# Kernel tuning notes

Hardware: AMD Instinct MI355X
Metric: run time of the kernel (lower is better)

## Reference

```python
import jax, jax.numpy as jnp
import numpy as np

N = 262144          # ray samples
L = 16              # grid levels
T = 2 ** 19         # hash table entries per level
F = 2               # features per entry
NMIN, NMAX = 16, 2048
SB = 1.0            # scene_bound
DW, CW = 64, 64     # density / color MLP widths

_PRIMES = jnp.array([1, 2654435761, 805459861], dtype=jnp.uint32)
_OFFS = jnp.asarray(np.stack(np.meshgrid([0, 1], [0, 1], [0, 1], indexing='ij'), -1).reshape(8, 3), dtype=jnp.uint32)  # 8 cube corners


def _scalings():
    g = np.exp((np.log(NMAX) - np.log(NMIN)) / (L - 1))
    return jnp.asarray(np.floor(NMIN * g ** np.arange(L)), dtype=jnp.float32)  # (L,)


def hash_encode(pos01, table):
    # pos01: (N,3) in [0,1]; table: (L*T, F)
    scaled = pos01[:, None, :] * _scalings()[None, :, None]        # (N,L,3)
    floor = jnp.floor(scaled)
    frac = scaled - floor                                          # (N,L,3)
    corners = floor.astype(jnp.uint32)[:, :, None, :] + _OFFS[None, None]  # (N,L,8,3)
    h = corners * _PRIMES                                          # uint32 wraparound hashing
    idx = (h[..., 0] ^ h[..., 1] ^ h[..., 2]) % jnp.uint32(T)      # (N,L,8)
    idx = idx.astype(jnp.int32) + (jnp.arange(L, dtype=jnp.int32) * T)[None, :, None]
    feats = table[idx]                                             # (N,L,8,F) gather
    sel = _OFFS.astype(bool)[None, None]                           # (1,1,8,3)
    w = jnp.prod(jnp.where(sel, frac[:, :, None, :], 1.0 - frac[:, :, None, :]), axis=-1)  # (N,L,8)
    out = jnp.einsum('nlcf,nlc->nlf', feats, w)                    # trilinear interp
    return out.reshape(out.shape[0], L * F)                        # (N, 32)


def sh_encode(d):
    # 4th-order real spherical harmonics, 16 components (instant-ngp convention)
    x, y, z = d[..., 0], d[..., 1], d[..., 2]
    xx, yy, zz = x * x, y * y, z * z
    xy, yz, xz = x * y, y * z, x * z
    return jnp.stack([
        jnp.full_like(x, 0.28209479177387814),
        -0.48860251190291987 * y,
        0.48860251190291987 * z,
        -0.48860251190291987 * x,
        1.0925484305920792 * xy,
        -1.0925484305920792 * yz,
        0.94617469575755997 * zz - 0.31539156525252005,
        -1.0925484305920792 * xz,
        0.54627421529603959 * (xx - yy),
        0.59004358992664352 * y * (-3.0 * xx + yy),
        2.8906114426405538 * xy * z,
        0.45704579946446572 * y * (1.0 - 5.0 * zz),
        0.3731763325901154 * z * (5.0 * zz - 3.0),
        0.45704579946446572 * x * (1.0 - 5.0 * zz),
        1.445305721320277 * z * (xx - yy),
        0.59004358992664352 * x * (xx - 3.0 * yy),
    ], axis=-1)  # (N,16)


def setup_inputs() -> dict:
    key = jax.random.key(0)
    ks = jax.random.split(key, 10)
    position = jax.random.uniform(ks[0], (N, 3), jnp.float32, -SB, SB)
    d = jax.random.normal(ks[1], (N, 3), jnp.float32)
    direction = d / jnp.linalg.norm(d, axis=-1, keepdims=True)
    hash_table = jax.random.uniform(ks[2], (L * T, F), jnp.float32, -1e-4, 1e-4)
    def dense(k, fin, fout, std):
        return (jax.random.normal(k, (fin, fout), jnp.float32) * std,
                jnp.zeros((fout,), jnp.float32))
    w1, b1 = dense(ks[3], L * F, DW, 0.01)      # normal() init in source
    w2, b2 = dense(ks[4], DW, 16, 0.01)
    w3, b3 = dense(ks[5], 16 + 16, CW, 0.01)
    w4, b4 = dense(ks[6], CW, CW, 0.01)
    w5, b5 = dense(ks[7], CW, 3, 0.1)           # default lecun-ish scale
    return dict(position=position, direction=direction, hash_table=hash_table,
                w1=w1, b1=b1, w2=w2, b2=b2, w3=w3, b3=b3, w4=w4, b4=b4, w5=w5, b5=b5)


def reference(position, direction, hash_table, w1, b1, w2, b2, w3, b3, w4, b4, w5, b5):
    p = (position + SB) / (2.0 * SB)                 # -> [0,1]
    enc = hash_encode(p, hash_table)                 # (N,32)
    h = jax.nn.relu(enc @ w1 + b1)                   # density MLP
    h = h @ w2 + b2                                  # (N,16)
    density = jnp.exp(h[:, 0:1])                     # exponential_density_activation
    sh = sh_encode(direction)                        # (N,16)
    c = jnp.concatenate([h, sh], axis=-1)            # (N,32)
    c = jax.nn.relu(c @ w3 + b3)
    c = jax.nn.relu(c @ w4 + b4)
    c = c @ w5 + b5
    color = jax.nn.sigmoid(c)                        # high_dynamic_range=False
    return jnp.concatenate([density, color], axis=-1)  # (N,4) drgbs
```

## Files before the change

### kernel.cpp

```cpp
#include <hip/hip_runtime.h>
#include <cmath>

namespace {
constexpr int kN = 262144;
constexpr int kL = 16;
constexpr int kT = 1 << 19;
constexpr unsigned kTMask = kT - 1;

typedef __attribute__((ext_vector_type(8))) short short8;
typedef __attribute__((ext_vector_type(4))) float f32x4;
typedef __attribute__((ext_vector_type(4))) unsigned short ushort4v;

struct Scales { float s[kL]; };

__device__ __forceinline__ unsigned short f2bf(float f) {
    unsigned u = __builtin_bit_cast(unsigned, f);
    return (unsigned short)((u + 0x7FFFu + ((u >> 16) & 1u)) >> 16);
}

__global__ __launch_bounds__(256) void prep_w(
    const float* __restrict__ w1, const float* __restrict__ w2,
    const float* __restrict__ w3, const float* __restrict__ w4,
    const float* __restrict__ w5, unsigned short* __restrict__ out)
{
    const int i = blockIdx.x * 256 + threadIdx.x;
    const int f = i >> 9;
    const int l = (i >> 3) & 63;
    const int e = i & 7;
    const int cl = l & 15;
    const int kg = l >> 4;
    float v = 0.0f;
    if (f < 4) {
        v = w1[(kg * 8 + e) * 64 + f * 16 + cl];
    } else if (f < 6) {
        const int q = f - 4;
        v = w2[(q * 32 + kg * 8 + e) * 16 + cl];
    } else if (f < 10) {
        v = w3[(kg * 8 + e) * 64 + (f - 6) * 16 + cl];
    } else if (f < 18) {
        const int g = f - 10, q = g >> 2, nt = g & 3;
        v = w4[(q * 32 + kg * 8 + e) * 64 + nt * 16 + cl];
    } else {
        const int q = f - 18;
        v = (cl < 3) ? w5[(q * 32 + kg * 8 + e) * 3 + cl] : 0.0f;
    }
    out[i] = f2bf(v);
}

__global__ __launch_bounds__(256) void ngp_encode(
    const float* __restrict__ pos,
    const float2* __restrict__ table,
    unsigned* __restrict__ enc,
    Scales sc)
{
    const int l = blockIdx.x >> 10;
    const int n = ((blockIdx.x & 1023) << 8) | threadIdx.x;

    const float s = sc.s[l];
    const float px = (pos[n * 3 + 0] + 1.0f) * 0.5f;
    const float py = (pos[n * 3 + 1] + 1.0f) * 0.5f;
    const float pz = (pos[n * 3 + 2] + 1.0f) * 0.5f;

    const float sx = px * s, sy = py * s, sz = pz * s;
    const float fx = floorf(sx), fy = floorf(sy), fz = floorf(sz);
    const float rx = sx - fx, ry = sy - fy, rz = sz - fz;
    const unsigned cx = (unsigned)fx, cy = (unsigned)fy, cz = (unsigned)fz;

    const unsigned hy0 = cy * 2654435761u, hy1 = (cy + 1u) * 2654435761u;
    const unsigned hz0 = cz * 805459861u,  hz1 = (cz + 1u) * 805459861u;
    const float2* __restrict__ tl = table + (size_t)l * kT;

    float2 f[8];
    #pragma unroll
    for (int c = 0; c < 8; ++c) {
        const unsigned ox = (c >> 2) & 1u, oy = (c >> 1) & 1u, oz = c & 1u;
        const unsigned h = (cx + ox) ^ (oy ? hy1 : hy0) ^ (oz ? hz1 : hz0);
        f[c] = tl[h & kTMask];
    }
    float f0 = 0.f, f1 = 0.f;
    #pragma unroll
    for (int c = 0; c < 8; ++c) {
        const unsigned ox = (c >> 2) & 1u, oy = (c >> 1) & 1u, oz = c & 1u;
        const float w = (ox ? rx : 1.f - rx) * (oy ? ry : 1.f - ry) * (oz ? rz : 1.f - rz);
        f0 = fmaf(f[c].x, w, f0);
        f1 = fmaf(f[c].y, w, f1);
    }
    enc[(size_t)l * kN + n] = (unsigned)f2bf(f0) | ((unsigned)f2bf(f1) << 16);
}

__global__ __launch_bounds__(256) void ngp_mlp_mfma(
    const unsigned* __restrict__ enc,
    const unsigned short* __restrict__ wbf,
    const float* __restrict__ dir,
    const float* __restrict__ b1, const float* __restrict__ b2,
    const float* __restrict__ b3, const float* __restrict__ b4,
    const float* __restrict__ b5,
    float* __restrict__ out)
{
    __shared__ unsigned short sA[4][4096];
    __shared__ unsigned short sB[4][2048];

    const int tid = threadIdx.x;
    const int wid = tid >> 6;
    const int l   = tid & 63;
    const int cl  = l & 15;
    const int kg  = l >> 4;
    unsigned short* __restrict__ A_ = sA[wid];
    unsigned short* __restrict__ B_ = sB[wid];
    const int gbase = blockIdx.x * 256 + wid * 64;

    {
        const int s = gbase + l;
        const float x = dir[s * 3 + 0], y = dir[s * 3 + 1], z = dir[s * 3 + 2];
        const float xx = x * x, yy = y * y, zz = z * z;
        const float xy = x * y, yz = y * z, xz = x * z;
        float sh[16];
        sh[0] = 0.28209479177387814f;
        sh[1] = -0.48860251190291987f * y;
        sh[2] = 0.48860251190291987f * z;
        sh[3] = -0.48860251190291987f * x;
        sh[4] = 1.0925484305920792f * xy;
        sh[5] = -1.0925484305920792f * yz;
        sh[6] = 0.94617469575755997f * zz - 0.31539156525252005f;
        sh[7] = -1.0925484305920792f * xz;
        sh[8] = 0.54627421529603959f * (xx - yy);
        sh[9] = 0.59004358992664352f * y * (-3.0f * xx + yy);
        sh[10] = 2.8906114426405538f * xy * z;
        sh[11] = 0.45704579946446572f * y * (1.0f - 5.0f * zz);
        sh[12] = 0.3731763325901154f * z * (5.0f * zz - 3.0f);
        sh[13] = 0.45704579946446572f * x * (1.0f - 5.0f * zz);
        sh[14] = 1.445305721320277f * z * (xx - yy);
        sh[15] = 0.59004358992664352f * x * (xx - 3.0f * yy);
        #pragma unroll
        for (int j = 0; j < 16; ++j)
            B_[(l >> 4) * 512 + (16 + j) * 16 + (l & 15)] = f2bf(sh[j]);
    }

    short8 A1[4];
    #pragma unroll
    for (int m = 0; m < 4; ++m) {
        #pragma unroll
        for (int j = 0; j < 4; ++j) {
            const unsigned v = enc[(size_t)(kg * 4 + j) * kN + (gbase + m * 16 + cl)];
            A1[m][2 * j]     = (short)(v & 0xFFFFu);
            A1[m][2 * j + 1] = (short)(v >> 16);
        }
    }
    {
        short8 B1[4];
        #pragma unroll
        for (int nt = 0; nt < 4; ++nt)
            B1[nt] = *reinterpret_cast<const short8*>(&wbf[(size_t)(nt) * 512 + l * 8]);

        f32x4 acc[4][4];
        #pragma unroll
        for (int nt = 0; nt < 4; ++nt) {
            const float bv = b1[nt * 16 + cl];
            #pragma unroll
            for (int m = 0; m < 4; ++m) {
                acc[m][nt][0] = bv; acc[m][nt][1] = bv; acc[m][nt][2] = bv; acc[m][nt][3] = bv;
            }
        }
        #pragma unroll
        for (int m = 0; m < 4; ++m)
            #pragma unroll
            for (int nt = 0; nt < 4; ++nt)
                acc[m][nt] = __builtin_amdgcn_mfma_f32_16x16x32_bf16(A1[m], B1[nt], acc[m][nt], 0, 0, 0);

        #pragma unroll
        for (int m = 0; m < 4; ++m) {
            #pragma unroll
            for (int nt = 0; nt < 4; ++nt) {
                ushort4v pk;
                #pragma unroll
                for (int r = 0; r < 4; ++r) pk[r] = f2bf(fmaxf(acc[m][nt][r], 0.0f));
                *reinterpret_cast<ushort4v*>(&A_[m * 1024 + (nt * 16 + cl) * 16 + kg * 4]) = pk;
            }
        }
    }

    {
        short8 A2[4][2];
        #pragma unroll
        for (int m = 0; m < 4; ++m)
            #pragma unroll
            for (int q = 0; q < 2; ++q)
                #pragma unroll
                for (int e = 0; e < 8; ++e)
                    A2[m][q][e] = (short)A_[m * 1024 + (q * 32 + kg * 8 + e) * 16 + cl];

        short8 B2[2];
        #pragma unroll
        for (int q = 0; q < 2; ++q)
            B2[q] = *reinterpret_cast<const short8*>(&wbf[(size_t)(4 + q) * 512 + l * 8]);

        f32x4 acc[4];
        const float bv = b2[cl];
        #pragma unroll
        for (int m = 0; m < 4; ++m) { acc[m][0] = bv; acc[m][1] = bv; acc[m][2] = bv; acc[m][3] = bv; }
        #pragma unroll
        for (int m = 0; m < 4; ++m)
            #pragma unroll
            for (int q = 0; q < 2; ++q)
                acc[m] = __builtin_amdgcn_mfma_f32_16x16x32_bf16(A2[m][q], B2[q], acc[m], 0, 0, 0);

        #pragma unroll
        for (int m = 0; m < 4; ++m) {
            if (cl == 0) {
                #pragma unroll
                for (int r = 0; r < 4; ++r)
                    out[(size_t)(gbase + m * 16 + kg * 4 + r) * 4 + 0] = expf(acc[m][r]);
            }
            ushort4v pk;
            #pragma unroll
            for (int r = 0; r < 4; ++r) pk[r] = f2bf(acc[m][r]);
            *reinterpret_cast<ushort4v*>(&B_[m * 512 + cl * 16 + kg * 4]) = pk;
        }
    }

    {
        short8 A3[4];
        #pragma unroll
        for (int m = 0; m < 4; ++m)
            #pragma unroll
            for (int e = 0; e < 8; ++e)
                A3[m][e] = (short)B_[m * 512 + (kg * 8 + e) * 16 + cl];

        short8 B3[4];
        #pragma unroll
        for (int nt = 0; nt < 4; ++nt)
            B3[nt] = *reinterpret_cast<const short8*>(&wbf[(size_t)(6 + nt) * 512 + l * 8]);

        f32x4 acc[4][4];
        #pragma unroll
        for (int nt = 0; nt < 4; ++nt) {
            const float bv = b3[nt * 16 + cl];
            #pragma unroll
            for (int m = 0; m < 4; ++m) {
                acc[m][nt][0] = bv; acc[m][nt][1] = bv; acc[m][nt][2] = bv; acc[m][nt][3] = bv;
            }
        }
        #pragma unroll
        for (int m = 0; m < 4; ++m)
            #pragma unroll
            for (int nt = 0; nt < 4; ++nt)
                acc[m][nt] = __builtin_amdgcn_mfma_f32_16x16x32_bf16(A3[m], B3[nt], acc[m][nt], 0, 0, 0);

        #pragma unroll
        for (int m = 0; m < 4; ++m) {
            #pragma unroll
            for (int nt = 0; nt < 4; ++nt) {
                ushort4v pk;
                #pragma unroll
                for (int r = 0; r < 4; ++r) pk[r] = f2bf(fmaxf(acc[m][nt][r], 0.0f));
                *reinterpret_cast<ushort4v*>(&A_[m * 1024 + (nt * 16 + cl) * 16 + kg * 4]) = pk;
            }
        }
    }

    {
        short8 A4[4][2];
        #pragma unroll
        for (int m = 0; m < 4; ++m)
            #pragma unroll
            for (int q = 0; q < 2; ++q)
                #pragma unroll
                for (int e = 0; e < 8; ++e)
                    A4[m][q][e] = (short)A_[m * 1024 + (q * 32 + kg * 8 + e) * 16 + cl];

        short8 B4[2][4];
        #pragma unroll
        for (int q = 0; q < 2; ++q)
            #pragma unroll
            for (int nt = 0; nt < 4; ++nt)
                B4[q][nt] = *reinterpret_cast<const short8*>(&wbf[(size_t)(10 + q * 4 + nt) * 512 + l * 8]);

        f32x4 acc[4][4];
        #pragma unroll
        for (int nt = 0; nt < 4; ++nt) {
            const float bv = b4[nt * 16 + cl];
            #pragma unroll
            for (int m = 0; m < 4; ++m) {
                acc[m][nt][0] = bv; acc[m][nt][1] = bv; acc[m][nt][2] = bv; acc[m][nt][3] = bv;
            }
        }
        #pragma unroll
        for (int m = 0; m < 4; ++m)
            #pragma unroll
            for (int nt = 0; nt < 4; ++nt)
                #pragma unroll
                for (int q = 0; q < 2; ++q)
                    acc[m][nt] = __builtin_amdgcn_mfma_f32_16x16x32_bf16(A4[m][q], B4[q][nt], acc[m][nt], 0, 0, 0);

        #pragma unroll
        for (int m = 0; m < 4; ++m) {
            #pragma unroll
            for (int nt = 0; nt < 4; ++nt) {
                ushort4v pk;
                #pragma unroll
                for (int r = 0; r < 4; ++r) pk[r] = f2bf(fmaxf(acc[m][nt][r], 0.0f));
                *reinterpret_cast<ushort4v*>(&A_[m * 1024 + (nt * 16 + cl) * 16 + kg * 4]) = pk;
            }
        }
    }

    {
        short8 A5[4][2];
        #pragma unroll
        for (int m = 0; m < 4; ++m)
            #pragma unroll
            for (int q = 0; q < 2; ++q)
                #pragma unroll
                for (int e = 0; e < 8; ++e)
                    A5[m][q][e] = (short)A_[m * 1024 + (q * 32 + kg * 8 + e) * 16 + cl];

        short8 B5[2];
        #pragma unroll
        for (int q = 0; q < 2; ++q)
            B5[q] = *reinterpret_cast<const short8*>(&wbf[(size_t)(18 + q) * 512 + l * 8]);

        f32x4 acc[4];
        const float bv = (cl < 3) ? b5[cl] : 0.0f;
        #pragma unroll
        for (int m = 0; m < 4; ++m) { acc[m][0] = bv; acc[m][1] = bv; acc[m][2] = bv; acc[m][3] = bv; }
        #pragma unroll
        for (int m = 0; m < 4; ++m)
            #pragma unroll
            for (int q = 0; q < 2; ++q)
                acc[m] = __builtin_amdgcn_mfma_f32_16x16x32_bf16(A5[m][q], B5[q], acc[m], 0, 0, 0);

        if (cl < 3) {
            #pragma unroll
            for (int m = 0; m < 4; ++m)
                #pragma unroll
                for (int r = 0; r < 4; ++r)
                    out[(size_t)(gbase + m * 16 + kg * 4 + r) * 4 + 1 + cl] =
                        1.0f / (1.0f + expf(-acc[m][r]));
        }
    }
}

}

extern "C" void kernel_launch(void* const* d_in, const int* in_sizes, int n_in,
                              void* d_out, int out_size, void* d_ws, size_t ws_size,
                              hipStream_t stream) {
    (void)in_sizes; (void)n_in; (void)out_size; (void)ws_size;

    Scales sc;
    const double g = exp((log(2048.0) - log(16.0)) / 15.0);
    for (int l = 0; l < kL; ++l) sc.s[l] = (float)floor(16.0 * pow(g, (double)l));

    const float*  pos   = (const float*)d_in[0];
    const float*  dir   = (const float*)d_in[1];
    const float2* table = (const float2*)d_in[2];
    const float *w1 = (const float*)d_in[3],  *b1 = (const float*)d_in[4];
    const float *w2 = (const float*)d_in[5],  *b2 = (const float*)d_in[6];
    const float *w3 = (const float*)d_in[7],  *b3 = (const float*)d_in[8];
    const float *w4 = (const float*)d_in[9],  *b4 = (const float*)d_in[10];
    const float *w5 = (const float*)d_in[11], *b5 = (const float*)d_in[12];
    float* out = (float*)d_out;

    unsigned short* wbf = (unsigned short*)d_ws;
    unsigned* enc = (unsigned*)((char*)d_ws + 32768);

    prep_w<<<40, 256, 0, stream>>>(w1, w2, w3, w4, w5, wbf);
    ngp_encode<<<kL * 1024, 256, 0, stream>>>(pos, table, enc, sc);
    ngp_mlp_mfma<<<kN / 256, 256, 0, stream>>>(enc, wbf, dir,
        b1, b2, b3, b4, b5, out);
}
```

Measured before the change: 166.3 us.

## Map hash levels to XCDs and process two samples per thread in encode

The encode kernel now remaps block IDs so each XCD (round-robin block placement across 8 dies) handles a single grid level at a time, keeping each level's hash table slice resident in that die's L2. Each thread now handles two samples, issuing 16 gathers before the interpolation to raise memory-level parallelism, and the grid is halved. Position loads and encoding stores use nontemporal hints to avoid polluting cache with streamed data. This relies on the hardware dispatching blocks round-robin across XCDs; if that assumption fails, locality gains vanish and register pressure rises.

```diff
diff --git a/kernel.cpp b/kernel.cpp
--- a/kernel.cpp
+++ b/kernel.cpp
@@ -53,39 +53,51 @@
     unsigned* __restrict__ enc,
     Scales sc)
 {
-    const int l = blockIdx.x >> 10;
-    const int n = ((blockIdx.x & 1023) << 8) | threadIdx.x;
+    const int bid = blockIdx.x;
+    const int xcd = bid & 7;
+    const int l = xcd + ((bid >> 12) << 3);
+    const int chunk = (bid >> 3) & 511;
+    const int n0 = (chunk << 9) | threadIdx.x;
 
     const float s = sc.s[l];
-    const float px = (pos[n * 3 + 0] + 1.0f) * 0.5f;
-    const float py = (pos[n * 3 + 1] + 1.0f) * 0.5f;
-    const float pz = (pos[n * 3 + 2] + 1.0f) * 0.5f;
-
-    const float sx = px * s, sy = py * s, sz = pz * s;
-    const float fx = floorf(sx), fy = floorf(sy), fz = floorf(sz);
-    const float rx = sx - fx, ry = sy - fy, rz = sz - fz;
-    const unsigned cx = (unsigned)fx, cy = (unsigned)fy, cz = (unsigned)fz;
-
-    const unsigned hy0 = cy * 2654435761u, hy1 = (cy + 1u) * 2654435761u;
-    const unsigned hz0 = cz * 805459861u,  hz1 = (cz + 1u) * 805459861u;
     const float2* __restrict__ tl = table + (size_t)l * kT;
 
-    float2 f[8];
+    float2 f[2][8];
+    float rx[2], ry[2], rz[2];
+
     #pragma unroll
-    for (int c = 0; c < 8; ++c) {
-        const unsigned ox = (c >> 2) & 1u, oy = (c >> 1) & 1u, oz = c & 1u;
-        const unsigned h = (cx + ox) ^ (oy ? hy1 : hy0) ^ (oz ? hz1 : hz0);
-        f[c] = tl[h & kTMask];
-    }
-    float f0 = 0.f, f1 = 0.f;
+    for (int t = 0; t < 2; ++t) {
+        const int n = n0 + t * 256;
+        const float px = (__builtin_nontemporal_load(&pos[n * 3 + 0]) + 1.0f) * 0.5f;
+        const float py = (__builtin_nontemporal_load(&pos[n * 3 + 1]) + 1.0f) * 0.5f;
+        const float pz = (__builtin_nontemporal_load(&pos[n * 3 + 2]) + 1.0f) * 0.5f;
+        const float sx = px * s, sy = py * s, sz = pz * s;
+        const float fx = floorf(sx), fy = floorf(sy), fz = floorf(sz);
+        rx[t] = sx - fx; ry[t] = sy - fy; rz[t] = sz - fz;
+        const unsigned cx = (unsigned)fx, cy = (unsigned)fy, cz = (unsigned)fz;
+        const unsigned hy0 = cy * 2654435761u, hy1 = (cy + 1u) * 2654435761u;
+        const unsigned hz0 = cz * 805459861u,  hz1 = (cz + 1u) * 805459861u;
+        #pragma unroll
+        for (int c = 0; c < 8; ++c) {
+            const unsigned ox = (c >> 2) & 1u, oy = (c >> 1) & 1u, oz = c & 1u;
+            const unsigned h = (cx + ox) ^ (oy ? hy1 : hy0) ^ (oz ? hz1 : hz0);
+            f[t][c] = tl[h & kTMask];
+        }
+    }
+
     #pragma unroll
-    for (int c = 0; c < 8; ++c) {
-        const unsigned ox = (c >> 2) & 1u, oy = (c >> 1) & 1u, oz = c & 1u;
-        const float w = (ox ? rx : 1.f - rx) * (oy ? ry : 1.f - ry) * (oz ? rz : 1.f - rz);
-        f0 = fmaf(f[c].x, w, f0);
-        f1 = fmaf(f[c].y, w, f1);
-    }
-    enc[(size_t)l * kN + n] = (unsigned)f2bf(f0) | ((unsigned)f2bf(f1) << 16);
+    for (int t = 0; t < 2; ++t) {
+        float f0 = 0.f, f1 = 0.f;
+        #pragma unroll
+        for (int c = 0; c < 8; ++c) {
+            const unsigned ox = (c >> 2) & 1u, oy = (c >> 1) & 1u, oz = c & 1u;
+            const float w = (ox ? rx[t] : 1.f - rx[t]) * (oy ? ry[t] : 1.f - ry[t]) * (oz ? rz[t] : 1.f - rz[t]);
+            f0 = fmaf(f[t][c].x, w, f0);
+            f1 = fmaf(f[t][c].y, w, f1);
+        }
+        const unsigned packed = (unsigned)f2bf(f0) | ((unsigned)f2bf(f1) << 16);
+        __builtin_nontemporal_store(packed, &enc[(size_t)l * kN + (n0 + t * 256)]);
+    }
 }
 
 __global__ __launch_bounds__(256) void ngp_mlp_mfma(
@@ -365,7 +377,7 @@
     unsigned* enc = (unsigned*)((char*)d_ws + 32768);
 
     prep_w<<<40, 256, 0, stream>>>(w1, w2, w3, w4, w5, wbf);
-    ngp_encode<<<kL * 1024, 256, 0, stream>>>(pos, table, enc, sc);
+    ngp_encode<<<8192, 256, 0, stream>>>(pos, table, enc, sc);
     ngp_mlp_mfma<<<kN / 256, 256, 0, stream>>>(enc, wbf, dir,
         b1, b2, b3, b4, b5, out);
 }
```

After: 177.0 us. 1.06x slower.
